# Performance work log

Hardware: AMD Instinct MI355X
Metric: run time of the kernel (lower is better)

Reference implementation:

```python
import jax, jax.numpy as jnp
import numpy as np
import math

EMBED_DIM = 256
NUM_HEADS = 8
NUM_LEVELS = 4
NUM_POINTS = 4
HEAD_DIM = EMBED_DIM // NUM_HEADS
SPATIAL_SHAPES = np.array([[100, 100], [50, 50], [25, 25], [13, 13]], dtype=np.int64)
LEN_V = int((SPATIAL_SHAPES[:, 0] * SPATIAL_SHAPES[:, 1]).sum())  # 13294
BS, LEN_Q = 8, 1024


def _grid_sample_bilinear(img, grid):
    """img: [N, C, H, W]; grid: [N, Hg, Wg, 2] in [-1,1].
    bilinear, padding_mode='zeros', align_corners=False. Returns [N, Hg, Wg, C]."""
    N, C, H, W = img.shape
    x = (grid[..., 0] + 1.0) * (W * 0.5) - 0.5
    y = (grid[..., 1] + 1.0) * (H * 0.5) - 0.5
    x0 = jnp.floor(x)
    y0 = jnp.floor(y)
    x1 = x0 + 1.0
    y1 = y0 + 1.0
    wx1 = x - x0
    wx0 = 1.0 - wx1
    wy1 = y - y0
    wy0 = 1.0 - wy1
    b = jnp.arange(N)[:, None, None]

    def gather(yi, xi):
        valid = (yi >= 0) & (yi <= H - 1) & (xi >= 0) & (xi <= W - 1)
        yc = jnp.clip(yi, 0, H - 1).astype(jnp.int32)
        xc = jnp.clip(xi, 0, W - 1).astype(jnp.int32)
        v = img[b, :, yc, xc]  # [N, Hg, Wg, C]
        return v * valid[..., None].astype(img.dtype)

    out = (gather(y0, x0) * (wy0 * wx0)[..., None]
           + gather(y0, x1) * (wy0 * wx1)[..., None]
           + gather(y1, x0) * (wy1 * wx0)[..., None]
           + gather(y1, x1) * (wy1 * wx1)[..., None])
    return out


def _offset_bias_init():
    # Faithful to _reset_parameters: per-head directional grid init for offsets bias.
    thetas = np.arange(NUM_HEADS, dtype=np.float32) * (2.0 * math.pi / NUM_HEADS)
    g = np.stack([np.cos(thetas), np.sin(thetas)], -1)
    g = g / np.abs(g).max(-1, keepdims=True)
    g = np.tile(g.reshape(NUM_HEADS, 1, 1, 2), (1, NUM_LEVELS, NUM_POINTS, 1))
    g = g * np.arange(1, NUM_POINTS + 1, dtype=np.float32).reshape(1, 1, -1, 1)
    return jnp.asarray(g.reshape(-1))


def setup_inputs() -> dict:
    key = jax.random.key(0)
    ks = jax.random.split(key, 8)
    TP = NUM_HEADS * NUM_LEVELS * NUM_POINTS  # 128

    def xavier(k, fan_in, fan_out):
        lim = math.sqrt(6.0 / (fan_in + fan_out))
        return jax.random.uniform(k, (fan_in, fan_out), jnp.float32, -lim, lim)

    return {
        "query": jax.random.normal(ks[0], (BS, LEN_Q, EMBED_DIM), jnp.float32),
        "reference_points": jax.random.uniform(ks[1], (BS, LEN_Q, NUM_LEVELS, 2), jnp.float32),
        "value": jax.random.normal(ks[2], (BS, LEN_V, EMBED_DIM), jnp.float32),
        "value_spatial_shapes": SPATIAL_SHAPES,
        # small random weights (instead of the zero-init) so the math paths are exercised
        "so_w": 0.01 * jax.random.normal(ks[3], (EMBED_DIM, TP * 2), jnp.float32),
        "so_b": _offset_bias_init(),
        "aw_w": 0.01 * jax.random.normal(ks[4], (EMBED_DIM, TP), jnp.float32),
        "aw_b": jnp.zeros((TP,), jnp.float32),
        "vp_w": xavier(ks[5], EMBED_DIM, EMBED_DIM),
        "vp_b": jnp.zeros((EMBED_DIM,), jnp.float32),
        "op_w": xavier(ks[6], EMBED_DIM, EMBED_DIM),
        "op_b": jnp.zeros((EMBED_DIM,), jnp.float32),
    }


def reference(query, reference_points, value, value_spatial_shapes,
              so_w, so_b, aw_w, aw_b, vp_w, vp_b, op_w, op_b):
    shapes = np.asarray(value_spatial_shapes)  # static python ints
    bs, len_q, D = query.shape
    H, L, P, hd = NUM_HEADS, NUM_LEVELS, NUM_POINTS, HEAD_DIM

    v = value @ vp_w + vp_b                              # [bs, len_v, D]
    v = v.reshape(bs, -1, H, hd)                         # [bs, len_v, H, hd]

    so = (query @ so_w + so_b).reshape(bs, len_q, H, L, P, 2)
    aw = (query @ aw_w + aw_b).reshape(bs, len_q, H, L * P)
    aw = jax.nn.softmax(aw, axis=-1).reshape(bs, len_q, H, L, P)

    # reference_points last dim == 2 branch: normalize offsets by (w, h) per level
    norm = jnp.asarray(shapes[:, ::-1].copy(), dtype=query.dtype).reshape(1, 1, 1, L, 1, 2)
    loc = reference_points.reshape(bs, len_q, 1, L, 1, 2) + so / norm
    grids = 2.0 * loc - 1.0                              # [bs, len_q, H, L, P, 2]
    grids = grids.transpose(0, 2, 1, 3, 4, 5).reshape(bs * H, len_q, L, P, 2)

    samples = []
    start = 0
    for lvl in range(L):
        h, w = int(shapes[lvl, 0]), int(shapes[lvl, 1])
        vl = v[:, start:start + h * w]                   # [bs, hw, H, hd]
        start += h * w
        img = vl.transpose(0, 2, 3, 1).reshape(bs * H, hd, h, w)
        s = _grid_sample_bilinear(img, grids[:, :, lvl])  # [bs*H, len_q, P, hd]
        samples.append(s)
    samp = jnp.stack(samples, axis=2)                    # [bs*H, len_q, L, P, hd]

    w_ = aw.transpose(0, 2, 1, 3, 4).reshape(bs * H, len_q, L, P)
    out = jnp.einsum('nqlpd,nqlp->nqd', samp, w_)        # [bs*H, len_q, hd]
    out = out.reshape(bs, H, len_q, hd).transpose(0, 2, 1, 3).reshape(bs, len_q, D)
    return out @ op_w + op_b
```

## Files before the change

### kernel.cpp

```cpp
#include <hip/hip_runtime.h>
#include <hip/hip_bf16.h>
#include <math.h>

#define BSZ 8
#define LQ  1024
#define LV  13294
#define NH  8
#define HD  32
#define VM  (BSZ * LV)
#define MQ  (BSZ * LQ)

typedef __attribute__((ext_vector_type(8))) short bf16x8;
typedef __attribute__((ext_vector_type(4))) float f32x4;

__device__ static inline unsigned short f2bf(float f) {
    unsigned int u = __float_as_uint(f);
    unsigned int r = (u + 0x7FFFu + ((u >> 16) & 1u)) >> 16;
    return (unsigned short)r;
}
__device__ static inline float bf2f(unsigned short s) {
    return __uint_as_float(((unsigned int)s) << 16);
}
__device__ static inline unsigned int pk2bf(float a, float b) {
    __hip_bfloat162 h = __float22bfloat162_rn(make_float2(a, b));
    return *(unsigned int*)&h;
}

__global__ __launch_bounds__(256) void prep_kernel(
    const float* __restrict__ vp_w, const float* __restrict__ op_w,
    const float* __restrict__ so_w, const float* __restrict__ aw_w,
    const float* __restrict__ query,
    unsigned short* __restrict__ wTv, unsigned short* __restrict__ wTo,
    unsigned short* __restrict__ wTso, unsigned short* __restrict__ wTaw,
    unsigned short* __restrict__ qhi, unsigned short* __restrict__ qlo)
{
    const int blk = blockIdx.x;
    const int t   = threadIdx.x;
    if (blk < 768) {
        const int n = blk & 255;
        const int k = t;
        const float* w; unsigned short* o;
        if      (blk < 256) { w = vp_w; o = wTv; }
        else if (blk < 512) { w = op_w; o = wTo; }
        else                { w = so_w; o = wTso; }
        o[(((k >> 5) * 256 + n) << 5) + (k & 31)] = f2bf(w[k * 256 + n]);
    } else if (blk < 896) {
        const int n = blk - 768;
        const int k = t;
        wTaw[(((k >> 5) * 128 + n) << 5) + (k & 31)] = f2bf(aw_w[k * 128 + n]);
    } else {
        const int idx = (blk - 896) * 256 + t;
        const float4 f = *(const float4*)(query + (size_t)idx * 4);
        ushort4 hi, lo;
        hi.x = f2bf(f.x); lo.x = f2bf(f.x - bf2f(hi.x));
        hi.y = f2bf(f.y); lo.y = f2bf(f.y - bf2f(hi.y));
        hi.z = f2bf(f.z); lo.z = f2bf(f.z - bf2f(hi.z));
        hi.w = f2bf(f.w); lo.w = f2bf(f.w - bf2f(hi.w));
        *(ushort4*)(qhi + (size_t)idx * 4) = hi;
        *(ushort4*)(qlo + (size_t)idx * 4) = lo;
    }
}

__global__ __launch_bounds__(256, 8) void vproj_mfma_kernel(
    const float* __restrict__ A,
    const unsigned short* __restrict__ wT,
    const float* __restrict__ bias,
    unsigned short* __restrict__ v)
{
    __shared__ __align__(16) unsigned short Asb[32 * 256];

    const int tid  = threadIdx.x;
    const int w    = tid >> 6;
    const int lane = tid & 63;
    const int mrow = lane & 15;
    const int quad = lane >> 4;
    const int m0   = blockIdx.x * 32;

#pragma unroll
    for (int r = 0; r < 8; ++r) {
        const int flat = r * 256 + tid;
        const int grow = flat >> 6;
        const int gcol = flat & 63;
        int gm = m0 + grow; if (gm >= VM) gm = VM - 1;
        const float4 f = *(const float4*)(A + (size_t)gm * 256 + gcol * 4);
        uint2 pk;
        pk.x = pk2bf(f.x, f.y);
        pk.y = pk2bf(f.z, f.w);
        const int c  = gcol >> 1;
        const int cp = c ^ (grow & 31);
        *(uint2*)&Asb[grow * 256 + cp * 8 + (gcol & 1) * 4] = pk;
    }
    __syncthreads();

    f32x4 acc[2][4];
#pragma unroll
    for (int i = 0; i < 2; ++i)
#pragma unroll
        for (int j = 0; j < 4; ++j) acc[i][j] = (f32x4)0.f;

#pragma unroll
    for (int kc = 0; kc < 8; ++kc) {
        bf16x8 wfr[4], af[2];
#pragma unroll
        for (int j = 0; j < 4; ++j) {
            const int n = w * 64 + j * 16 + mrow;
            wfr[j] = *(const bf16x8*)(const void*)(wT + (((size_t)kc * 256 + n) << 5) + quad * 8);
        }
#pragma unroll
        for (int i = 0; i < 2; ++i) {
            const int mr = i * 16 + mrow;
            const int cp = (kc * 4 + quad) ^ (mr & 31);
            af[i] = *(const bf16x8*)(const void*)&Asb[mr * 256 + cp * 8];
        }
#pragma unroll
        for (int i = 0; i < 2; ++i)
#pragma unroll
            for (int j = 0; j < 4; ++j)
                acc[i][j] = __builtin_amdgcn_mfma_f32_16x16x32_bf16(
                    wfr[j], af[i], acc[i][j], 0, 0, 0);
    }

    float4 bj[4];
#pragma unroll
    for (int j = 0; j < 4; ++j)
        bj[j] = *(const float4*)(bias + w * 64 + j * 16 + quad * 4);

#pragma unroll
    for (int i = 0; i < 2; ++i) {
        const int gm = m0 + i * 16 + mrow;
        if (gm >= VM) continue;
        const unsigned int b   = (unsigned int)gm / (unsigned int)LV;
        const unsigned int pix = (unsigned int)gm - b * (unsigned int)LV;
#pragma unroll
        for (int j = 0; j < 4; ++j) {
            const int ch = w * 64 + j * 16 + quad * 4;
            const int h  = ch >> 5, cc = ch & 31;
            uint2 o;
            o.x = pk2bf(acc[i][j][0] + bj[j].x, acc[i][j][1] + bj[j].y);
            o.y = pk2bf(acc[i][j][2] + bj[j].z, acc[i][j][3] + bj[j].w);
            *(uint2*)(v + (((size_t)(b * NH + h)) * LV + pix) * HD + cc) = o;
        }
    }
}

template<int NJ, bool SPLIT>
__global__ __launch_bounds__(256) void gemm16_kernel(
    const unsigned short* __restrict__ A,
    const unsigned short* __restrict__ A2,
    const unsigned short* __restrict__ wT,
    const float* __restrict__ bias,
    float* __restrict__ C)
{
    constexpr int N = NJ * 64;
    __shared__ __align__(16) unsigned short Ah[16 * 256];
    __shared__ __align__(16) unsigned short Al[SPLIT ? 16 * 256 : 8];

    const int tid  = threadIdx.x;
    const int w    = tid >> 6;
    const int lane = tid & 63;
    const int mrow = lane & 15;
    const int quad = lane >> 4;
    const int m0   = blockIdx.x * 16;

#pragma unroll
    for (int r = 0; r < 2; ++r) {
        const int flat = r * 256 + tid;
        const int row  = flat >> 5;
        const int ck   = flat & 31;
        const int cp   = ck ^ row;
        *(uint4*)&Ah[row * 256 + cp * 8] =
            *(const uint4*)(A + (size_t)(m0 + row) * 256 + ck * 8);
        if (SPLIT)
            *(uint4*)&Al[row * 256 + cp * 8] =
                *(const uint4*)(A2 + (size_t)(m0 + row) * 256 + ck * 8);
    }
    __syncthreads();

    f32x4 acc[NJ];
#pragma unroll
    for (int j = 0; j < NJ; ++j) acc[j] = (f32x4)0.f;

#pragma unroll
    for (int kc = 0; kc < 8; ++kc) {
        bf16x8 wf[NJ];
#pragma unroll
        for (int j = 0; j < NJ; ++j) {
            const int n = w * (NJ * 16) + j * 16 + mrow;
            wf[j] = *(const bf16x8*)(const void*)(wT + (((size_t)kc * N + n) << 5) + quad * 8);
        }
        const int cp = (kc * 4 + quad) ^ mrow;
        const bf16x8 af = *(const bf16x8*)(const void*)&Ah[mrow * 256 + cp * 8];
#pragma unroll
        for (int j = 0; j < NJ; ++j)
            acc[j] = __builtin_amdgcn_mfma_f32_16x16x32_bf16(wf[j], af, acc[j], 0, 0, 0);
        if (SPLIT) {
            const bf16x8 af2 = *(const bf16x8*)(const void*)&Al[mrow * 256 + cp * 8];
#pragma unroll
            for (int j = 0; j < NJ; ++j)
                acc[j] = __builtin_amdgcn_mfma_f32_16x16x32_bf16(wf[j], af2, acc[j], 0, 0, 0);
        }
    }

    const int gm = m0 + mrow;
#pragma unroll
    for (int j = 0; j < NJ; ++j) {
        const int col = w * (NJ * 16) + j * 16 + quad * 4;
        const float4 bb = *(const float4*)(bias + col);
        float4 o;
        o.x = acc[j][0] + bb.x;
        o.y = acc[j][1] + bb.y;
        o.z = acc[j][2] + bb.z;
        o.w = acc[j][3] + bb.w;
        *(float4*)(C + (size_t)gm * N + col) = o;
    }
}

__global__ __launch_bounds__(256) void sample_kernel(
    const unsigned short* __restrict__ v,
    const float* __restrict__ so_raw,
    const float* __restrict__ aw_raw,
    const float* __restrict__ refp,
    unsigned short* __restrict__ out_head)
{
    const int blk = blockIdx.x;
    const int xcd = blk & 7;
    const int j   = blk >> 3;
    const int bh  = xcd * 8 + (j >> 8);
    const int qg  = j & 255;
    const int b   = bh >> 3;
    const int h   = bh & 7;

    const int wv   = threadIdx.x >> 6;
    const int lane = threadIdx.x & 63;
    const int ch   = lane & 7;
    const int pz   = lane >> 3;

    const int q  = qg * 4 + wv;
    const int rq = b * LQ + q;

    const float l0 = aw_raw[rq * 128 + h * 16 + pz];
    const float l1 = aw_raw[rq * 128 + h * 16 + 8 + pz];
    float mx = fmaxf(l0, l1);
    mx = fmaxf(mx, __shfl_xor(mx, 8));
    mx = fmaxf(mx, __shfl_xor(mx, 16));
    mx = fmaxf(mx, __shfl_xor(mx, 32));
    const float e0 = __expf(l0 - mx), e1 = __expf(l1 - mx);
    float sm = e0 + e1;
    sm += __shfl_xor(sm, 8);
    sm += __shfl_xor(sm, 16);
    sm += __shfl_xor(sm, 32);
    const float inv_s = 1.f / sm;

    const unsigned short* vb = v + (size_t)bh * (LV * HD) + ch * 4;

    float a0 = 0.f, a1 = 0.f, a2 = 0.f, a3 = 0.f;

#pragma unroll
    for (int r = 0; r < 2; ++r) {
        const int pt = r * 8 + pz;
        const int l  = pt >> 2;
        const int p  = pt & 3;
        const float wgt = (r ? e1 : e0) * inv_s;

        const int Wl = (l == 0) ? 100 : (l == 1) ? 50 : (l == 2) ? 25 : 13;
        const int st = (l == 0) ? 0 : (l == 1) ? 10000 : (l == 2) ? 12500 : 13125;
        const float invW = (l == 0) ? 0.01f : (l == 1) ? 0.02f : (l == 2) ? 0.04f
                                            : (1.0f / 13.0f);
        const float fw = (float)Wl;

        const float2 rxy = *(const float2*)(refp + (size_t)rq * 8 + l * 2);
        const float2 sxy = *(const float2*)(so_raw + (size_t)rq * 256 + h * 32 + l * 8 + p * 2);

        const float x = (rxy.x + sxy.x * invW) * fw - 0.5f;
        const float y = (rxy.y + sxy.y * invW) * fw - 0.5f;

        const float xf = floorf(x), yf = floorf(y);
        const int x0 = (int)xf, y0 = (int)yf;
        const float wx1 = x - xf, wx0 = 1.f - wx1;
        const float wy1 = y - yf, wy0 = 1.f - wy1;

        const float vx0 = (x0 >= 0 && x0 < Wl) ? 1.f : 0.f;
        const float vx1 = (x0 + 1 >= 0 && x0 + 1 < Wl) ? 1.f : 0.f;
        const float vy0 = (y0 >= 0 && y0 < Wl) ? 1.f : 0.f;
        const float vy1 = (y0 + 1 >= 0 && y0 + 1 < Wl) ? 1.f : 0.f;

        const int xc0 = min(max(x0, 0), Wl - 1);
        const int xc1 = min(max(x0 + 1, 0), Wl - 1);
        const int yc0 = min(max(y0, 0), Wl - 1);
        const int yc1 = min(max(y0 + 1, 0), Wl - 1);

        const float w00 = wgt * wy0 * wx0 * vy0 * vx0;
        const float w01 = wgt * wy0 * wx1 * vy0 * vx1;
        const float w10 = wgt * wy1 * wx0 * vy1 * vx0;
        const float w11 = wgt * wy1 * wx1 * vy1 * vx1;

        const int row0 = (st + yc0 * Wl) * HD;
        const int row1 = (st + yc1 * Wl) * HD;

        const ushort4 u00 = *(const ushort4*)(vb + row0 + xc0 * HD);
        const ushort4 u01 = *(const ushort4*)(vb + row0 + xc1 * HD);
        const ushort4 u10 = *(const ushort4*)(vb + row1 + xc0 * HD);
        const ushort4 u11 = *(const ushort4*)(vb + row1 + xc1 * HD);

        a0 = fmaf(w00, bf2f(u00.x), a0);
        a1 = fmaf(w00, bf2f(u00.y), a1);
        a2 = fmaf(w00, bf2f(u00.z), a2);
        a3 = fmaf(w00, bf2f(u00.w), a3);
        a0 = fmaf(w01, bf2f(u01.x), a0);
        a1 = fmaf(w01, bf2f(u01.y), a1);
        a2 = fmaf(w01, bf2f(u01.z), a2);
        a3 = fmaf(w01, bf2f(u01.w), a3);
        a0 = fmaf(w10, bf2f(u10.x), a0);
        a1 = fmaf(w10, bf2f(u10.y), a1);
        a2 = fmaf(w10, bf2f(u10.z), a2);
        a3 = fmaf(w10, bf2f(u10.w), a3);
        a0 = fmaf(w11, bf2f(u11.x), a0);
        a1 = fmaf(w11, bf2f(u11.y), a1);
        a2 = fmaf(w11, bf2f(u11.z), a2);
        a3 = fmaf(w11, bf2f(u11.w), a3);
    }

    a0 += __shfl_xor(a0, 8);  a1 += __shfl_xor(a1, 8);
    a2 += __shfl_xor(a2, 8);  a3 += __shfl_xor(a3, 8);
    a0 += __shfl_xor(a0, 16); a1 += __shfl_xor(a1, 16);
    a2 += __shfl_xor(a2, 16); a3 += __shfl_xor(a3, 16);
    a0 += __shfl_xor(a0, 32); a1 += __shfl_xor(a1, 32);
    a2 += __shfl_xor(a2, 32); a3 += __shfl_xor(a3, 32);

    if (pz == 0) {
        uint2 o;
        o.x = pk2bf(a0, a1);
        o.y = pk2bf(a2, a3);
        *(uint2*)(out_head + (size_t)rq * 256 + (h << 5) + (ch << 2)) = o;
    }
}

extern "C" void kernel_launch(void* const* d_in, const int* in_sizes, int n_in,
                              void* d_out, int out_size, void* d_ws, size_t ws_size,
                              hipStream_t stream)
{
    const float* query = (const float*)d_in[0];
    const float* refp  = (const float*)d_in[1];
    const float* value = (const float*)d_in[2];
    const float* so_w  = (const float*)d_in[4];
    const float* so_b  = (const float*)d_in[5];
    const float* aw_w  = (const float*)d_in[6];
    const float* aw_b  = (const float*)d_in[7];
    const float* vp_w  = (const float*)d_in[8];
    const float* vp_b  = (const float*)d_in[9];
    const float* op_w  = (const float*)d_in[10];
    const float* op_b  = (const float*)d_in[11];
    float* out = (float*)d_out;

    float* ws = (float*)d_ws;
    size_t off = 0;
    unsigned short* v = (unsigned short*)(ws + off);
    off += (size_t)BSZ * NH * LV * HD / 2;
    unsigned short* wTv  = (unsigned short*)(ws + off); off += 32768;
    unsigned short* wTo  = (unsigned short*)(ws + off); off += 32768;
    unsigned short* wTso = (unsigned short*)(ws + off); off += 32768;
    unsigned short* wTaw = (unsigned short*)(ws + off); off += 16384;
    unsigned short* qhi  = (unsigned short*)(ws + off); off += (size_t)MQ * 128;
    unsigned short* qlo  = (unsigned short*)(ws + off); off += (size_t)MQ * 128;
    float* so_raw = ws + off; off += (size_t)MQ * 256;
    float* aw_raw = ws + off; off += (size_t)MQ * 128;
    unsigned short* out_head = (unsigned short*)(ws + off);
    off += (size_t)MQ * 128;

    prep_kernel<<<2944, 256, 0, stream>>>(vp_w, op_w, so_w, aw_w, query,
                                          wTv, wTo, wTso, wTaw, qhi, qlo);

    vproj_mfma_kernel<<<(VM + 31) / 32, 256, 0, stream>>>(value, wTv, vp_b, v);

    gemm16_kernel<4, true><<<MQ / 16, 256, 0, stream>>>(qhi, qlo, wTso, so_b, so_raw);
    gemm16_kernel<2, true><<<MQ / 16, 256, 0, stream>>>(qhi, qlo, wTaw, aw_b, aw_raw);

    sample_kernel<<<BSZ * NH * LQ / 4, 256, 0, stream>>>(
        v, so_raw, aw_raw, refp, out_head);

    gemm16_kernel<4, false><<<MQ / 16, 256, 0, stream>>>(out_head, nullptr, wTo, op_b, out);
}
```

Baseline: 291.2 us.

## Fuse value projection with offset and attention-weight GEMMs into one launch

Merges the value-projection GEMM and the two query-side GEMMs into a single kernel whose blocks branch on block index. This removes two launches and lets the small GEMMs fill the tail of the large one. The value-projection tile grows from 32 to 64 rows, with a larger LDS buffer and occupancy lowered to 4 waves per SIMD. The sample kernel's XCD-aware block remapping is dropped in favour of a plain linear mapping, which may hurt L2 locality across chiplets.

```diff
diff --git a/kernel.cpp b/kernel.cpp
--- a/kernel.cpp
+++ b/kernel.cpp
@@ -9,6 +9,7 @@
 #define HD  32
 #define VM  (BSZ * LV)
 #define MQ  (BSZ * LQ)
+#define NVB ((VM + 63) / 64)
 
 typedef __attribute__((ext_vector_type(8))) short bf16x8;
 typedef __attribute__((ext_vector_type(4))) float f32x4;
@@ -61,23 +62,110 @@
     }
 }
 
-__global__ __launch_bounds__(256, 8) void vproj_mfma_kernel(
-    const float* __restrict__ A,
-    const unsigned short* __restrict__ wT,
-    const float* __restrict__ bias,
-    unsigned short* __restrict__ v)
-{
-    __shared__ __align__(16) unsigned short Asb[32 * 256];
+template<int NJ, bool SPLIT>
+__device__ __forceinline__ void gemm16_body(
+    unsigned short* __restrict__ lds,
+    const unsigned short* __restrict__ A, const unsigned short* __restrict__ A2,
+    const unsigned short* __restrict__ wT, const float* __restrict__ bias,
+    float* __restrict__ C, int m0)
+{
+    constexpr int N = NJ * 64;
+    unsigned short* Ah = lds;
+    unsigned short* Al = lds + 16 * 256;
 
     const int tid  = threadIdx.x;
     const int w    = tid >> 6;
     const int lane = tid & 63;
     const int mrow = lane & 15;
     const int quad = lane >> 4;
-    const int m0   = blockIdx.x * 32;
-
-#pragma unroll
-    for (int r = 0; r < 8; ++r) {
+
+#pragma unroll
+    for (int r = 0; r < 2; ++r) {
+        const int flat = r * 256 + tid;
+        const int row  = flat >> 5;
+        const int ck   = flat & 31;
+        const int cp   = ck ^ row;
+        *(uint4*)&Ah[row * 256 + cp * 8] =
+            *(const uint4*)(A + (size_t)(m0 + row) * 256 + ck * 8);
+        if (SPLIT)
+            *(uint4*)&Al[row * 256 + cp * 8] =
+                *(const uint4*)(A2 + (size_t)(m0 + row) * 256 + ck * 8);
+    }
+    __syncthreads();
+
+    f32x4 acc[NJ];
+#pragma unroll
+    for (int j = 0; j < NJ; ++j) acc[j] = (f32x4)0.f;
+
+#pragma unroll
+    for (int kc = 0; kc < 8; ++kc) {
+        bf16x8 wf[NJ];
+#pragma unroll
+        for (int j = 0; j < NJ; ++j) {
+            const int n = w * (NJ * 16) + j * 16 + mrow;
+            wf[j] = *(const bf16x8*)(const void*)(wT + (((size_t)kc * N + n) << 5) + quad * 8);
+        }
+        const int cp = (kc * 4 + quad) ^ mrow;
+        const bf16x8 af = *(const bf16x8*)(const void*)&Ah[mrow * 256 + cp * 8];
+#pragma unroll
+        for (int j = 0; j < NJ; ++j)
+            acc[j] = __builtin_amdgcn_mfma_f32_16x16x32_bf16(wf[j], af, acc[j], 0, 0, 0);
+        if (SPLIT) {
+            const bf16x8 af2 = *(const bf16x8*)(const void*)&Al[mrow * 256 + cp * 8];
+#pragma unroll
+            for (int j = 0; j < NJ; ++j)
+                acc[j] = __builtin_amdgcn_mfma_f32_16x16x32_bf16(wf[j], af2, acc[j], 0, 0, 0);
+        }
+    }
+
+    const int gm = m0 + mrow;
+#pragma unroll
+    for (int j = 0; j < NJ; ++j) {
+        const int col = w * (NJ * 16) + j * 16 + quad * 4;
+        const float4 bb = *(const float4*)(bias + col);
+        float4 o;
+        o.x = acc[j][0] + bb.x;
+        o.y = acc[j][1] + bb.y;
+        o.z = acc[j][2] + bb.z;
+        o.w = acc[j][3] + bb.w;
+        *(float4*)(C + (size_t)gm * N + col) = o;
+    }
+}
+
+__global__ __launch_bounds__(256, 4) void fused1_kernel(
+    const float* __restrict__ A,
+    const unsigned short* __restrict__ wTv,
+    const float* __restrict__ vp_b,
+    unsigned short* __restrict__ v,
+    const unsigned short* __restrict__ qhi,
+    const unsigned short* __restrict__ qlo,
+    const unsigned short* __restrict__ wTso, const float* __restrict__ so_b,
+    float* __restrict__ so_raw,
+    const unsigned short* __restrict__ wTaw, const float* __restrict__ aw_b,
+    float* __restrict__ aw_raw)
+{
+    __shared__ __align__(16) unsigned short lds_u16[64 * 256];
+
+    const int blk = blockIdx.x;
+    if (blk >= NVB) {
+        if (blk < NVB + 512)
+            gemm16_body<4, true>(lds_u16, qhi, qlo, wTso, so_b, so_raw,
+                                 (blk - NVB) * 16);
+        else
+            gemm16_body<2, true>(lds_u16, qhi, qlo, wTaw, aw_b, aw_raw,
+                                 (blk - NVB - 512) * 16);
+        return;
+    }
+
+    const int tid  = threadIdx.x;
+    const int w    = tid >> 6;
+    const int lane = tid & 63;
+    const int mrow = lane & 15;
+    const int quad = lane >> 4;
+    const int m0   = blk * 64;
+
+#pragma unroll
+    for (int r = 0; r < 16; ++r) {
         const int flat = r * 256 + tid;
         const int grow = flat >> 6;
         const int gcol = flat & 63;
@@ -88,32 +176,32 @@
         pk.y = pk2bf(f.z, f.w);
         const int c  = gcol >> 1;
         const int cp = c ^ (grow & 31);
-        *(uint2*)&Asb[grow * 256 + cp * 8 + (gcol & 1) * 4] = pk;
+        *(uint2*)&lds_u16[grow * 256 + cp * 8 + (gcol & 1) * 4] = pk;
     }
     __syncthreads();
 
-    f32x4 acc[2][4];
-#pragma unroll
-    for (int i = 0; i < 2; ++i)
+    f32x4 acc[4][4];
+#pragma unroll
+    for (int i = 0; i < 4; ++i)
 #pragma unroll
         for (int j = 0; j < 4; ++j) acc[i][j] = (f32x4)0.f;
 
 #pragma unroll
     for (int kc = 0; kc < 8; ++kc) {
-        bf16x8 wfr[4], af[2];
+        bf16x8 wfr[4], af[4];
 #pragma unroll
         for (int j = 0; j < 4; ++j) {
             const int n = w * 64 + j * 16 + mrow;
-            wfr[j] = *(const bf16x8*)(const void*)(wT + (((size_t)kc * 256 + n) << 5) + quad * 8);
+            wfr[j] = *(const bf16x8*)(const void*)(wTv + (((size_t)kc * 256 + n) << 5) + quad * 8);
         }
 #pragma unroll
-        for (int i = 0; i < 2; ++i) {
+        for (int i = 0; i < 4; ++i) {
             const int mr = i * 16 + mrow;
             const int cp = (kc * 4 + quad) ^ (mr & 31);
-            af[i] = *(const bf16x8*)(const void*)&Asb[mr * 256 + cp * 8];
+            af[i] = *(const bf16x8*)(const void*)&lds_u16[mr * 256 + cp * 8];
         }
 #pragma unroll
-        for (int i = 0; i < 2; ++i)
+        for (int i = 0; i < 4; ++i)
 #pragma unroll
             for (int j = 0; j < 4; ++j)
                 acc[i][j] = __builtin_amdgcn_mfma_f32_16x16x32_bf16(
@@ -123,10 +211,10 @@
     float4 bj[4];
 #pragma unroll
     for (int j = 0; j < 4; ++j)
-        bj[j] = *(const float4*)(bias + w * 64 + j * 16 + quad * 4);
-
-#pragma unroll
-    for (int i = 0; i < 2; ++i) {
+        bj[j] = *(const float4*)(vp_b + w * 64 + j * 16 + quad * 4);
+
+#pragma unroll
+    for (int i = 0; i < 4; ++i) {
         const int gm = m0 + i * 16 + mrow;
         if (gm >= VM) continue;
         const unsigned int b   = (unsigned int)gm / (unsigned int)LV;
@@ -143,76 +231,14 @@
     }
 }
 
-template<int NJ, bool SPLIT>
-__global__ __launch_bounds__(256) void gemm16_kernel(
-    const unsigned short* __restrict__ A,
-    const unsigned short* __restrict__ A2,
-    const unsigned short* __restrict__ wT,
+__global__ __launch_bounds__(256) void oproj_kernel(
+    const unsigned short* __restrict__ Ah,
+    const unsigned short* __restrict__ wTo,
     const float* __restrict__ bias,
     float* __restrict__ C)
 {
-    constexpr int N = NJ * 64;
-    __shared__ __align__(16) unsigned short Ah[16 * 256];
-    __shared__ __align__(16) unsigned short Al[SPLIT ? 16 * 256 : 8];
-
-    const int tid  = threadIdx.x;
-    const int w    = tid >> 6;
-    const int lane = tid & 63;
-    const int mrow = lane & 15;
-    const int quad = lane >> 4;
-    const int m0   = blockIdx.x * 16;
-
-#pragma unroll
-    for (int r = 0; r < 2; ++r) {
-        const int flat = r * 256 + tid;
-        const int row  = flat >> 5;
-        const int ck   = flat & 31;
-        const int cp   = ck ^ row;
-        *(uint4*)&Ah[row * 256 + cp * 8] =
-            *(const uint4*)(A + (size_t)(m0 + row) * 256 + ck * 8);
-        if (SPLIT)
-            *(uint4*)&Al[row * 256 + cp * 8] =
-                *(const uint4*)(A2 + (size_t)(m0 + row) * 256 + ck * 8);
-    }
-    __syncthreads();
-
-    f32x4 acc[NJ];
-#pragma unroll
-    for (int j = 0; j < NJ; ++j) acc[j] = (f32x4)0.f;
-
-#pragma unroll
-    for (int kc = 0; kc < 8; ++kc) {
-        bf16x8 wf[NJ];
-#pragma unroll
-        for (int j = 0; j < NJ; ++j) {
-            const int n = w * (NJ * 16) + j * 16 + mrow;
-            wf[j] = *(const bf16x8*)(const void*)(wT + (((size_t)kc * N + n) << 5) + quad * 8);
-        }
-        const int cp = (kc * 4 + quad) ^ mrow;
-        const bf16x8 af = *(const bf16x8*)(const void*)&Ah[mrow * 256 + cp * 8];
-#pragma unroll
-        for (int j = 0; j < NJ; ++j)
-            acc[j] = __builtin_amdgcn_mfma_f32_16x16x32_bf16(wf[j], af, acc[j], 0, 0, 0);
-        if (SPLIT) {
-            const bf16x8 af2 = *(const bf16x8*)(const void*)&Al[mrow * 256 + cp * 8];
-#pragma unroll
-            for (int j = 0; j < NJ; ++j)
-                acc[j] = __builtin_amdgcn_mfma_f32_16x16x32_bf16(wf[j], af2, acc[j], 0, 0, 0);
-        }
-    }
-
-    const int gm = m0 + mrow;
-#pragma unroll
-    for (int j = 0; j < NJ; ++j) {
-        const int col = w * (NJ * 16) + j * 16 + quad * 4;
-        const float4 bb = *(const float4*)(bias + col);
-        float4 o;
-        o.x = acc[j][0] + bb.x;
-        o.y = acc[j][1] + bb.y;
-        o.z = acc[j][2] + bb.z;
-        o.w = acc[j][3] + bb.w;
-        *(float4*)(C + (size_t)gm * N + col) = o;
-    }
+    __shared__ __align__(16) unsigned short lds_u16[16 * 256];
+    gemm16_body<4, false>(lds_u16, Ah, nullptr, wTo, bias, C, blockIdx.x * 16);
 }
 
 __global__ __launch_bounds__(256) void sample_kernel(
@@ -223,10 +249,8 @@
     unsigned short* __restrict__ out_head)
 {
     const int blk = blockIdx.x;
-    const int xcd = blk & 7;
-    const int j   = blk >> 3;
-    const int bh  = xcd * 8 + (j >> 8);
-    const int qg  = j & 255;
+    const int bh  = blk >> 8;
+    const int j2  = blk & 255;
     const int b   = bh >> 3;
     const int h   = bh & 7;
 
@@ -235,7 +259,7 @@
     const int ch   = lane & 7;
     const int pz   = lane >> 3;
 
-    const int q  = qg * 4 + wv;
+    const int q  = j2 * 4 + wv;
     const int rq = b * LQ + q;
 
     const float l0 = aw_raw[rq * 128 + h * 16 + pz];
@@ -370,13 +394,11 @@
     prep_kernel<<<2944, 256, 0, stream>>>(vp_w, op_w, so_w, aw_w, query,
                                           wTv, wTo, wTso, wTaw, qhi, qlo);
 
-    vproj_mfma_kernel<<<(VM + 31) / 32, 256, 0, stream>>>(value, wTv, vp_b, v);
-
-    gemm16_kernel<4, true><<<MQ / 16, 256, 0, stream>>>(qhi, qlo, wTso, so_b, so_raw);
-    gemm16_kernel<2, true><<<MQ / 16, 256, 0, stream>>>(qhi, qlo, wTaw, aw_b, aw_raw);
+    fused1_kernel<<<NVB + 1024, 256, 0, stream>>>(
+        value, wTv, vp_b, v, qhi, qlo, wTso, so_b, so_raw, wTaw, aw_b, aw_raw);
 
     sample_kernel<<<BSZ * NH * LQ / 4, 256, 0, stream>>>(
         v, so_raw, aw_raw, refp, out_head);
 
-    gemm16_kernel<4, false><<<MQ / 16, 256, 0, stream>>>(out_head, nullptr, wTo, op_b, out);
-}
+    oproj_kernel<<<MQ / 16, 256, 0, stream>>>(out_head, wTo, op_b, out);
+}
```

Result: faster. 247.8 us (-14.9%).
